# Kernel optimization log

Hardware: AMD Instinct MI355X
Metric: run time of the kernel (lower is better)

## Reference

```python
import jax, jax.numpy as jnp
import numpy as np

B, T, QL, KVL, D, H = 4, 512, 2, 1, 1024, 16
N = T * QL          # query tokens for self-attn
HD = D // H
MLP_H = 4 * D
EPS_ADA = 1e-6
EPS_LN = 1e-5
NEG = -10000.0


def _ln(x, eps):
    mu = jnp.mean(x, axis=-1, keepdims=True)
    xc = x - mu
    var = jnp.mean(xc * xc, axis=-1, keepdims=True)
    return xc * jax.lax.rsqrt(var + eps)


def _attention(xq, xk, xv, wq, wk, wv, wo, bo, mask, pad_add):
    # xq:[B,Nq,D] xk/xv:[B,Nk,D]; mask:[Nq,Nk] bool; pad_add:[B,1,1,Nk]
    qh = (xq @ wq).reshape(B, -1, H, HD).transpose(0, 2, 1, 3)
    kh = (xk @ wk).reshape(B, -1, H, HD).transpose(0, 2, 1, 3)
    vh = (xv @ wv).reshape(B, -1, H, HD).transpose(0, 2, 1, 3)
    dots = jnp.einsum('bhnd,bhmd->bhnm', qh, kh) * (HD ** -0.5)
    dots = jnp.where(mask[None, None], dots, jnp.asarray(NEG, dots.dtype))
    dots = dots + pad_add
    attn = jax.nn.softmax(dots, axis=-1)
    out = jnp.einsum('bhnm,bhmd->bhnd', attn, vh)
    out = out.transpose(0, 2, 1, 3).reshape(B, -1, D)
    return out @ wo + bo


def setup_inputs() -> dict:
    key = jax.random.key(0)
    ks = jax.random.split(key, 32)
    s = 0.02
    d = {
        'q': jax.random.normal(ks[0], (B, N, D), jnp.float32),
        'c': jax.random.normal(ks[1], (B, T, D), jnp.float32),
        'pe': jax.random.normal(ks[2], (B, T, D), jnp.float32),
        'padding_mask': jax.random.randint(ks[3], (B, T), 0, 2, jnp.int32),
        'w_mod': jax.random.normal(ks[4], (D, 6 * D), jnp.float32) * s,
        'b_mod': jnp.zeros((6 * D,), jnp.float32),
        'sa_wq': jax.random.normal(ks[5], (D, D), jnp.float32) * s,
        'sa_wk': jax.random.normal(ks[6], (D, D), jnp.float32) * s,
        'sa_wv': jax.random.normal(ks[7], (D, D), jnp.float32) * s,
        'sa_wo': jax.random.normal(ks[8], (D, D), jnp.float32) * s,
        'sa_bo': jnp.zeros((D,), jnp.float32),
        'ca_wq': jax.random.normal(ks[9], (D, D), jnp.float32) * s,
        'ca_wk': jax.random.normal(ks[10], (D, D), jnp.float32) * s,
        'ca_wv': jax.random.normal(ks[11], (D, D), jnp.float32) * s,
        'ca_wo': jax.random.normal(ks[12], (D, D), jnp.float32) * s,
        'ca_bo': jnp.zeros((D,), jnp.float32),
        'gk': jnp.ones((D,), jnp.float32), 'bk': jnp.zeros((D,), jnp.float32),
        'gv': jnp.ones((D,), jnp.float32), 'bv': jnp.zeros((D,), jnp.float32),
        'w_alpha': jax.random.normal(ks[13], (2 * D, D), jnp.float32) * s,
        'b_alpha': jnp.zeros((D,), jnp.float32),
        'w1': jax.random.normal(ks[14], (D, MLP_H), jnp.float32) * s,
        'b1': jnp.zeros((MLP_H,), jnp.float32),
        'w2': jax.random.normal(ks[15], (MLP_H, D), jnp.float32) * s,
        'b2': jnp.zeros((D,), jnp.float32),
    }
    return d


def reference(q, c, pe, padding_mask, w_mod, b_mod,
              sa_wq, sa_wk, sa_wv, sa_wo, sa_bo,
              ca_wq, ca_wk, ca_wv, ca_wo, ca_bo,
              gk, bk, gv, bv, w_alpha, b_alpha, w1, b1, w2, b2):
    # AdaLN modulation from condition c
    mod = jax.nn.silu(c) @ w_mod + b_mod                    # [B,T,6D]
    scale_sa, shift_sa, scale_ca, shift_ca, scale_mlp, shift_mlp = jnp.split(mod, 6, axis=2)
    rep = lambda t: jnp.repeat(t, QL, axis=1)               # [B,T,D]->[B,N,D]

    # masks
    causal = jnp.tril(jnp.ones((N, N), bool))
    tril_t = jnp.tril(jnp.ones((T, T), bool))
    cross_mask = jnp.repeat(jnp.repeat(tril_t, QL, axis=0), KVL, axis=1)  # [N, T*KVL]
    pad_f = padding_mask.astype(q.dtype)
    pad_sa = (jnp.repeat(pad_f, QL, axis=1) * NEG)[:, None, None, :]      # keys len N
    pad_ca = (jnp.repeat(pad_f, KVL, axis=1) * NEG)[:, None, None, :]     # keys len T

    # self-attention (pre-norm + modulation)
    q1 = _ln(q, EPS_ADA) * (1 + rep(scale_sa)) + rep(shift_sa)
    q1 = _attention(q1, q1, q1, sa_wq, sa_wk, sa_wv, sa_wo, sa_bo, causal, pad_sa)
    q = q1 + q

    # cross-attention with custom mask
    q2 = _ln(q, EPS_ADA) * (1 + rep(scale_ca)) + rep(shift_ca)
    kin = _ln(c + pe, EPS_LN) * gk + bk
    vin = _ln(c, EPS_LN) * gv + bv
    q2 = _attention(q2, kin, vin, ca_wq, ca_wk, ca_wv, ca_wo, ca_bo, cross_mask, pad_ca)
    alpha = jnp.concatenate([q2, q], axis=-1) @ w_alpha + b_alpha
    q = (1 + alpha) * q2 + q

    # MLP
    q3 = _ln(q, EPS_ADA) * (1 + rep(scale_mlp)) + rep(shift_mlp)
    h = jax.nn.gelu(q3 @ w1 + b1, approximate=False)
    q = q + (h @ w2 + b2)
    return q
```

## Files before the change

kernel.cpp:

```cpp
#include <hip/hip_runtime.h>
#include <cstdint>

typedef unsigned short u16;
typedef __attribute__((ext_vector_type(8))) short bf16x8;
typedef __attribute__((ext_vector_type(4))) float f32x4;

#define DEV static __device__ __forceinline__
#define AS1 __attribute__((address_space(1)))
#define AS3 __attribute__((address_space(3)))

static constexpr int Bb = 4, Tt = 512, Nn = 1024, Dd = 1024, Hh = 16;
static constexpr float NEGV = -10000.0f;

DEV u16 f2bf(float f) {
  unsigned int u = __builtin_bit_cast(unsigned int, f);
  u += 0x7fffu + ((u >> 16) & 1u);
  return (u16)(u >> 16);
}
DEV float bf2f(u16 s) {
  unsigned int u = ((unsigned int)s) << 16;
  return __builtin_bit_cast(float, u);
}
DEV f32x4 mfma16(bf16x8 a, bf16x8 b, f32x4 c) {
  return __builtin_amdgcn_mfma_f32_16x16x32_bf16(a, b, c, 0, 0, 0);
}
DEV void gload16(const u16* g, u16* lds) {
  __builtin_amdgcn_global_load_lds((AS1 const unsigned int*)g, (AS3 unsigned int*)lds, 16, 0, 0);
}
DEV int swz8(int wg, int nwg) { const int c = nwg >> 3; return (wg & 7) * c + (wg >> 3); }

__global__ __launch_bounds__(256) void transpose_cast(const float* __restrict__ src,
                                                      u16* __restrict__ dst, int R, int C) {
  __shared__ float tile[32][33];
  const int c0 = blockIdx.x * 32, r0 = blockIdx.y * 32;
  const int tx = threadIdx.x, ty = threadIdx.y;
#pragma unroll
  for (int j = 0; j < 4; ++j)
    tile[ty + 8 * j][tx] = src[(size_t)(r0 + ty + 8 * j) * C + c0 + tx];
  __syncthreads();
#pragma unroll
  for (int j = 0; j < 4; ++j)
    dst[(size_t)(c0 + ty + 8 * j) * R + r0 + tx] = f2bf(tile[tx][ty + 8 * j]);
}

__global__ __launch_bounds__(256) void silu_k(const float* __restrict__ c, u16* __restrict__ o, int n) {
  int i = blockIdx.x * 256 + threadIdx.x;
  if (i < n) { float x = c[i]; o[i] = f2bf(x / (1.0f + __expf(-x))); }
}

__global__ __launch_bounds__(256) void cat_k(const float* __restrict__ q2, const float* __restrict__ qr,
                                             u16* __restrict__ cat) {
  int i = blockIdx.x * 256 + threadIdx.x;
  int r = i >> 10, c = i & 1023;
  cat[(size_t)r * 2048 + c] = f2bf(q2[i]);
  cat[(size_t)r * 2048 + 1024 + c] = f2bf(qr[i]);
}

__global__ __launch_bounds__(256) void init_k(float* __restrict__ out, const float* __restrict__ bias,
                                              const float* __restrict__ res) {
  const int i = blockIdx.x * 256 + threadIdx.x;
  const float4 bv = ((const float4*)bias)[i & 255];
  float4 v = bv;
  if (res) {
    const float4 rv = ((const float4*)res)[i];
    v.x += rv.x; v.y += rv.y; v.z += rv.z; v.w += rv.w;
  }
  ((float4*)out)[i] = v;
}

__global__ __launch_bounds__(256) void comb_k(const float* __restrict__ alp, const float* __restrict__ q2,
                                              float* __restrict__ qres) {
  const int i = blockIdx.x * 256 + threadIdx.x;
  const float4 a = ((const float4*)alp)[i];
  const float4 b = ((const float4*)q2)[i];
  float4 r = ((float4*)qres)[i];
  r.x += (1.0f + a.x) * b.x; r.y += (1.0f + a.y) * b.y;
  r.z += (1.0f + a.z) * b.z; r.w += (1.0f + a.w) * b.w;
  ((float4*)qres)[i] = r;
}

__global__ __launch_bounds__(64) void mrow_k(const int* __restrict__ pm, float* __restrict__ M) {
  const int tid = threadIdx.x;
  const int b = tid >> 4, seg = tid & 15;
  int pre[32];
  int a = 1;
#pragma unroll
  for (int j = 0; j < 32; ++j) { a &= pm[b * 512 + seg * 32 + j]; pre[j] = a; }
  const int total = a;
  int excl = 1;
  for (int s = 0; s < 16; ++s) {
    int o = __shfl(total, (b << 4) + s, 64);
    if (s < seg) excl &= o;
  }
#pragma unroll
  for (int j = 0; j < 32; ++j)
    M[b * 512 + seg * 32 + j] = (excl & pre[j]) ? NEGV : 0.0f;
}

__global__ __launch_bounds__(256) void ln_mod_k(const float* __restrict__ X, const u16* __restrict__ MOD,
                                                u16* __restrict__ OUT, int chunk) {
  const int row = blockIdx.x;
  const int b = row >> 10, i = row & 1023, t = i >> 1;
  const int tid = threadIdx.x;
  const float4 xv = *(const float4*)&X[(size_t)row * 1024 + tid * 4];
  float s = xv.x + xv.y + xv.z + xv.w;
  float q = xv.x * xv.x + xv.y * xv.y + xv.z * xv.z + xv.w * xv.w;
#pragma unroll
  for (int off = 32; off > 0; off >>= 1) { s += __shfl_down(s, off); q += __shfl_down(q, off); }
  __shared__ float rs[4], rq[4];
  if ((tid & 63) == 0) { rs[tid >> 6] = s; rq[tid >> 6] = q; }
  __syncthreads();
  float S = rs[0] + rs[1] + rs[2] + rs[3];
  float Q = rq[0] + rq[1] + rq[2] + rq[3];
  const float mu = S * (1.0f / 1024.0f);
  const float var = Q * (1.0f / 1024.0f) - mu * mu;
  const float rstd = rsqrtf(var + 1e-6f);
  const u16* mrow = MOD + (size_t)(b * Tt + t) * 6144 + chunk * 1024 + tid * 4;
  u16* out = OUT + (size_t)row * 1024 + tid * 4;
  const float xx[4] = {xv.x, xv.y, xv.z, xv.w};
#pragma unroll
  for (int j = 0; j < 4; ++j) {
    float sc = bf2f(mrow[j]);
    float sh = bf2f(mrow[1024 + j]);
    out[j] = f2bf((xx[j] - mu) * rstd * (1.0f + sc) + sh);
  }
}

__global__ __launch_bounds__(256) void ln_kv_k(const float* __restrict__ C_, const float* __restrict__ PE,
                                               const float* __restrict__ gk, const float* __restrict__ bk,
                                               const float* __restrict__ gv, const float* __restrict__ bv,
                                               u16* __restrict__ KIN, u16* __restrict__ VIN) {
  const int row = blockIdx.x, tid = threadIdx.x;
  const size_t base = (size_t)row * 1024 + tid * 4;
  const float4 cv = *(const float4*)&C_[base];
  const float4 pv = *(const float4*)&PE[base];
  const float a[4] = {cv.x + pv.x, cv.y + pv.y, cv.z + pv.z, cv.w + pv.w};
  const float bb[4] = {cv.x, cv.y, cv.z, cv.w};
  float sa = a[0] + a[1] + a[2] + a[3];
  float qa = a[0] * a[0] + a[1] * a[1] + a[2] * a[2] + a[3] * a[3];
  float sb = bb[0] + bb[1] + bb[2] + bb[3];
  float qb = bb[0] * bb[0] + bb[1] * bb[1] + bb[2] * bb[2] + bb[3] * bb[3];
#pragma unroll
  for (int off = 32; off > 0; off >>= 1) {
    sa += __shfl_down(sa, off); qa += __shfl_down(qa, off);
    sb += __shfl_down(sb, off); qb += __shfl_down(qb, off);
  }
  __shared__ float r4[4][4];
  if ((tid & 63) == 0) {
    int w = tid >> 6;
    r4[0][w] = sa; r4[1][w] = qa; r4[2][w] = sb; r4[3][w] = qb;
  }
  __syncthreads();
  sa = r4[0][0] + r4[0][1] + r4[0][2] + r4[0][3];
  qa = r4[1][0] + r4[1][1] + r4[1][2] + r4[1][3];
  sb = r4[2][0] + r4[2][1] + r4[2][2] + r4[2][3];
  qb = r4[3][0] + r4[3][1] + r4[3][2] + r4[3][3];
  const float mua = sa * (1.0f / 1024.0f);
  const float ra = rsqrtf(qa * (1.0f / 1024.0f) - mua * mua + 1e-5f);
  const float mub = sb * (1.0f / 1024.0f);
  const float rb = rsqrtf(qb * (1.0f / 1024.0f) - mub * mub + 1e-5f);
#pragma unroll
  for (int j = 0; j < 4; ++j) {
    int d = tid * 4 + j;
    KIN[(size_t)row * 1024 + d] = f2bf((a[j] - mua) * ra * gk[d] + bk[d]);
    VIN[(size_t)row * 1024 + d] = f2bf((bb[j] - mub) * rb * gv[d] + bv[d]);
  }
}

DEV void stage32(const u16* __restrict__ A, const u16* __restrict__ Bt, int K,
                 int brow, int bcol, int kb, u16 (*As)[32], u16 (*Bs)[32]) {
  const int l = threadIdx.x & 63, wid = threadIdx.x >> 6;
#pragma unroll
  for (int p = 0; p < 2; ++p) {
    const int r0 = p * 64 + wid * 16;
    const int row = r0 + (l >> 2), kof = (l & 3) << 3;
    gload16(&A[(size_t)(brow + row) * K + kb + kof], &As[r0][0]);
    gload16(&Bt[(size_t)(bcol + row) * K + kb + kof], &Bs[r0][0]);
  }
}

DEV void gcore(const u16* __restrict__ A, const u16* __restrict__ Bt, int K,
               int brow, int bcol, int k0, int nk32,
               u16 (*As)[128][32], u16 (*Bs)[128][32], f32x4 (&acc)[4][4]) {
  const int l = threadIdx.x & 63, wid = threadIdx.x >> 6;
  const int wr = wid >> 1, wc = wid & 1;
  const int fr = l & 15, fg = l >> 4;
  stage32(A, Bt, K, brow, bcol, k0, As[0], Bs[0]);
  __syncthreads();
  int cur = 0;
  for (int kt = 0; kt < nk32; ++kt) {
    if (kt + 1 < nk32)
      stage32(A, Bt, K, brow, bcol, k0 + ((kt + 1) << 5), As[cur ^ 1], Bs[cur ^ 1]);
    bf16x8 af[4], bfr[4];
#pragma unroll
    for (int m = 0; m < 4; ++m) af[m] = *(const bf16x8*)&As[cur][wr * 64 + m * 16 + fr][fg * 8];
#pragma unroll
    for (int n = 0; n < 4; ++n) bfr[n] = *(const bf16x8*)&Bs[cur][wc * 64 + n * 16 + fr][fg * 8];
#pragma unroll
    for (int m = 0; m < 4; ++m)
#pragma unroll
      for (int n = 0; n < 4; ++n) acc[m][n] = mfma16(af[m], bfr[n], acc[m][n]);
    __syncthreads();
    cur ^= 1;
  }
}

template <int EPI>
__global__ __launch_bounds__(256) void gemm_k(const u16* __restrict__ A, const u16* __restrict__ Bt,
                                              int N, int K, const float* __restrict__ bias,
                                              u16* __restrict__ outb, int nbx) {
  __shared__ u16 As[2][128][32];
  __shared__ u16 Bs[2][128][32];
  const int wg = swz8(blockIdx.x, gridDim.x);
  const int brow = (wg / nbx) * 128, bcol = (wg % nbx) * 128;
  const int l = threadIdx.x & 63, wid = threadIdx.x >> 6;
  const int wr = wid >> 1, wc = wid & 1, fr = l & 15, fg = l >> 4;
  f32x4 acc[4][4];
#pragma unroll
  for (int m = 0; m < 4; ++m)
#pragma unroll
    for (int n = 0; n < 4; ++n) acc[m][n] = (f32x4){0.f, 0.f, 0.f, 0.f};
  gcore(A, Bt, K, brow, bcol, 0, K >> 5, As, Bs, acc);
#pragma unroll
  for (int m = 0; m < 4; ++m)
#pragma unroll
    for (int n = 0; n < 4; ++n)
#pragma unroll
      for (int r = 0; r < 4; ++r) {
        const int row = brow + wr * 64 + m * 16 + fg * 4 + r;
        const int col = bcol + wc * 64 + n * 16 + fr;
        float v = acc[m][n][r];
        if (EPI != 0) v += bias[col];
        if (EPI == 2) {
          const float u = v * (0.7978845608f + 0.0356774081f * v * v);
          v = v / (1.0f + __expf(-2.0f * u));
        }
        outb[(size_t)row * N + col] = f2bf(v);
      }
}

__global__ __launch_bounds__(256) void gemm_sk(const u16* __restrict__ A, const u16* __restrict__ Bt,
                                               int N, int K, float* __restrict__ outf, int nbx) {
  __shared__ u16 As[2][128][32];
  __shared__ u16 Bs[2][128][32];
  const int wg = swz8(blockIdx.x, gridDim.x);
  const int brow = (wg / nbx) * 128, bcol = (wg % nbx) * 128;
  const int half32 = K >> 6;
  const int k0 = blockIdx.y * (half32 << 5);
  const int l = threadIdx.x & 63, wid = threadIdx.x >> 6;
  const int wr = wid >> 1, wc = wid & 1, fr = l & 15, fg = l >> 4;
  f32x4 acc[4][4];
#pragma unroll
  for (int m = 0; m < 4; ++m)
#pragma unroll
    for (int n = 0; n < 4; ++n) acc[m][n] = (f32x4){0.f, 0.f, 0.f, 0.f};
  gcore(A, Bt, K, brow, bcol, k0, half32, As, Bs, acc);
#pragma unroll
  for (int m = 0; m < 4; ++m)
#pragma unroll
    for (int n = 0; n < 4; ++n)
#pragma unroll
      for (int r = 0; r < 4; ++r) {
        const int row = brow + wr * 64 + m * 16 + fg * 4 + r;
        const int col = bcol + wc * 64 + n * 16 + fr;
        atomicAdd(&outf[(size_t)row * N + col], acc[m][n][r]);
      }
}

__global__ __launch_bounds__(256) void gemm3_k(const u16* A0, const u16* A1, const u16* A2,
                                               const u16* B0, const u16* B1, const u16* B2,
                                               u16* O0, u16* O1, u16* O2) {
  const int z = blockIdx.y;
  const int wg = swz8(blockIdx.x, gridDim.x);
  const int bx = wg & 7, by = wg >> 3;
  if (z > 0 && by >= 16) return;
  const u16* A = z == 0 ? A0 : (z == 1 ? A1 : A2);
  const u16* Bt = z == 0 ? B0 : (z == 1 ? B1 : B2);
  u16* O = z == 0 ? O0 : (z == 1 ? O1 : O2);
  __shared__ u16 As[2][128][32];
  __shared__ u16 Bs[2][128][32];
  const int brow = by * 128, bcol = bx * 128;
  const int l = threadIdx.x & 63, wid = threadIdx.x >> 6;
  const int wr = wid >> 1, wc = wid & 1, fr = l & 15, fg = l >> 4;
  f32x4 acc[4][4];
#pragma unroll
  for (int m = 0; m < 4; ++m)
#pragma unroll
    for (int n = 0; n < 4; ++n) acc[m][n] = (f32x4){0.f, 0.f, 0.f, 0.f};
  gcore(A, Bt, 1024, brow, bcol, 0, 32, As, Bs, acc);
#pragma unroll
  for (int m = 0; m < 4; ++m)
#pragma unroll
    for (int n = 0; n < 4; ++n)
#pragma unroll
      for (int r = 0; r < 4; ++r) {
        const int row = brow + wr * 64 + m * 16 + fg * 4 + r;
        const int col = bcol + wc * 64 + n * 16 + fr;
        O[(size_t)row * 1024 + col] = f2bf(acc[m][n][r]);
      }
}

template <int QDIV, int PDIV>
__global__ __launch_bounds__(256) void attn_k(const u16* __restrict__ QH, const u16* __restrict__ KH,
                                              const u16* __restrict__ VH, u16* __restrict__ AO,
                                              const int* __restrict__ pmask, const float* __restrict__ Mrow,
                                              int Nq, int Nk, int qs, int ks) {
  __shared__ u16 Ks[32][72];
  __shared__ u16 Vt[64][40];
  __shared__ u16 Pl[4][16][40];
  const int tid = threadIdx.x;
  const int l = tid & 63, wid = tid >> 6;
  const int fr = l & 15, fg = l >> 4;
  const int nqb = Nq >> 6;
  const int wgid = swz8(blockIdx.x, gridDim.x);
  const int qb = wgid % nqb;
  const int bh = wgid / nqb;
  const int h = bh & 15, b = bh >> 4;
  const int q0 = qb * 64 + wid * 16;

  const size_t qrow = (size_t)(b * Nq + q0 + fr) * qs + h * 64;
  const bf16x8 aq0 = *(const bf16x8*)&QH[qrow + fg * 8];
  const bf16x8 aq1 = *(const bf16x8*)&QH[qrow + 32 + fg * 8];

  float Mr[4];
#pragma unroll
  for (int r = 0; r < 4; ++r) Mr[r] = Mrow[b * Tt + ((q0 + fg * 4 + r) >> 1)];

  f32x4 o[4];
#pragma unroll
  for (int c = 0; c < 4; ++c) o[c] = (f32x4){0.f, 0.f, 0.f, 0.f};
  float lsum[4] = {0.f, 0.f, 0.f, 0.f};

  int nkt = Nk >> 5;
  if (Mrow[b * Tt + ((qb * 64) >> 1)] == 0.0f) {
    const int kallow = (qb * 64 + 63) / QDIV + 1;
    const int t = (kallow + 31) >> 5;
    if (t < nkt) nkt = t;
  }

  const int srow = tid >> 3, skof = (tid & 7) << 3;
  for (int kt = 0; kt < nkt; ++kt) {
    const int kb = kt << 5;
    {
      const size_t g = (size_t)(b * Nk + kb + srow) * ks + h * 64 + skof;
      *(uint4*)&Ks[srow][skof] = *(const uint4*)&KH[g];
      union { uint4 u; u16 s[8]; } uv;
      uv.u = *(const uint4*)&VH[g];
#pragma unroll
      for (int j = 0; j < 8; ++j) Vt[skof + j][srow] = uv.s[j];
    }
    __syncthreads();

    f32x4 s0 = (f32x4){0.f, 0.f, 0.f, 0.f}, s1 = (f32x4){0.f, 0.f, 0.f, 0.f};
    {
      bf16x8 kf;
      kf = *(const bf16x8*)&Ks[fr][fg * 8];        s0 = mfma16(aq0, kf, s0);
      kf = *(const bf16x8*)&Ks[fr][32 + fg * 8];   s0 = mfma16(aq1, kf, s0);
      kf = *(const bf16x8*)&Ks[16 + fr][fg * 8];       s1 = mfma16(aq0, kf, s1);
      kf = *(const bf16x8*)&Ks[16 + fr][32 + fg * 8];  s1 = mfma16(aq1, kf, s1);
    }
    const int c0 = kb + fr, c1 = kb + 16 + fr;
    const float pad0 = pmask[b * Tt + (PDIV == 2 ? (c0 >> 1) : c0)] ? NEGV : 0.0f;
    const float pad1 = pmask[b * Tt + (PDIV == 2 ? (c1 >> 1) : c1)] ? NEGV : 0.0f;

#pragma unroll
    for (int r = 0; r < 4; ++r) {
      const int rq = (q0 + fg * 4 + r) >> (QDIV == 2 ? 1 : 0);
      float v0 = s0[r] * 0.125f; v0 = (c0 <= rq) ? v0 : NEGV; v0 += pad0;
      float v1 = s1[r] * 0.125f; v1 = (c1 <= rq) ? v1 : NEGV; v1 += pad1;
      const float p0 = __expf(v0 - Mr[r]);
      const float p1 = __expf(v1 - Mr[r]);
      lsum[r] += p0 + p1;
      Pl[wid][fg * 4 + r][fr] = f2bf(p0);
      Pl[wid][fg * 4 + r][16 + fr] = f2bf(p1);
    }

    const bf16x8 pa = *(const bf16x8*)&Pl[wid][fr][fg * 8];
#pragma unroll
    for (int c = 0; c < 4; ++c) {
      const bf16x8 vb = *(const bf16x8*)&Vt[c * 16 + fr][fg * 8];
      o[c] = mfma16(pa, vb, o[c]);
    }
    __syncthreads();
  }

#pragma unroll
  for (int r = 0; r < 4; ++r) {
    lsum[r] += __shfl_xor(lsum[r], 1);
    lsum[r] += __shfl_xor(lsum[r], 2);
    lsum[r] += __shfl_xor(lsum[r], 4);
    lsum[r] += __shfl_xor(lsum[r], 8);
  }

#pragma unroll
  for (int c = 0; c < 4; ++c)
#pragma unroll
    for (int r = 0; r < 4; ++r) {
      const int row = q0 + fg * 4 + r;
      AO[(size_t)(b * Nq + row) * Dd + h * 64 + c * 16 + fr] = f2bf(o[c][r] / lsum[r]);
    }
}

extern "C" void kernel_launch(void* const* d_in, const int* in_sizes, int n_in,
                              void* d_out, int out_size, void* d_ws, size_t ws_size,
                              hipStream_t stream) {
  (void)in_sizes; (void)n_in; (void)out_size; (void)ws_size;
  const float* q_in   = (const float*)d_in[0];
  const float* c_in   = (const float*)d_in[1];
  const float* pe     = (const float*)d_in[2];
  const int*   pmask  = (const int*)d_in[3];
  const float* w_mod  = (const float*)d_in[4];
  const float* b_mod  = (const float*)d_in[5];
  const float* sa_wq  = (const float*)d_in[6];
  const float* sa_wk  = (const float*)d_in[7];
  const float* sa_wv  = (const float*)d_in[8];
  const float* sa_wo  = (const float*)d_in[9];
  const float* sa_bo  = (const float*)d_in[10];
  const float* ca_wq  = (const float*)d_in[11];
  const float* ca_wk  = (const float*)d_in[12];
  const float* ca_wv  = (const float*)d_in[13];
  const float* ca_wo  = (const float*)d_in[14];
  const float* ca_bo  = (const float*)d_in[15];
  const float* gk     = (const float*)d_in[16];
  const float* bk     = (const float*)d_in[17];
  const float* gv     = (const float*)d_in[18];
  const float* bv     = (const float*)d_in[19];
  const float* w_alpha= (const float*)d_in[20];
  const float* b_alpha= (const float*)d_in[21];
  const float* w1     = (const float*)d_in[22];
  const float* b1     = (const float*)d_in[23];
  const float* w2     = (const float*)d_in[24];
  const float* b2     = (const float*)d_in[25];

  u16* ws = (u16*)d_ws;
  u16* WMODt  = ws + 0;
  float* Mp   = (float*)WMODt;
  u16* SAWQt  = ws + 6291456;
  u16* SAWKt  = ws + 7340032;
  u16* SAWVt  = ws + 8388608;
  u16* SAWOt  = ws + 9437184;
  u16* CAWQt  = ws + 10485760;
  u16* CAWKt  = ws + 11534336;
  u16* CAWVt  = ws + 12582912;
  u16* CAWOt  = ws + 13631488;
  u16* WALPHt = ws + 14680064;
  u16* W1t    = ws + 16777216;
  u16* W2t    = ws + 20971520;
  u16* Xs     = ws + 25165824;
  u16* KINp   = Xs;
  u16* VINp   = SAWQt;
  u16* MODbf  = ws + 27262976;
  u16* LNO    = ws + 39845888;
  u16* BIG    = ws + 44040192;
  u16* QKVp = BIG;
  u16* AOp  = BIG + 12582912;
  u16* CAQp = BIG;
  u16* CAKp = BIG + 4194304;
  u16* CAVp = BIG + 6291456;
  u16* AO2p = BIG + 8388608;
  u16* CATp = BIG;
  float* ALPf = (float*)(BIG + 8388608);
  u16* HBp  = BIG;
  float* Qres = (float*)(ws + 60817408);
  float* Q2f  = Qres + 4194304;
  float* outp = (float*)d_out;

  const dim3 blk(256);
  auto TR = [&](const float* s, u16* d, int R, int C) {
    transpose_cast<<<dim3(C / 32, R / 32), dim3(32, 8), 0, stream>>>(s, d, R, C);
  };

  TR(w_mod, WMODt, 1024, 6144);
  TR(sa_wq, SAWQt, 1024, 1024); TR(sa_wk, SAWKt, 1024, 1024);
  TR(sa_wv, SAWVt, 1024, 1024); TR(sa_wo, SAWOt, 1024, 1024);
  TR(ca_wq, CAWQt, 1024, 1024); TR(ca_wk, CAWKt, 1024, 1024);
  TR(ca_wv, CAWVt, 1024, 1024); TR(ca_wo, CAWOt, 1024, 1024);
  TR(w_alpha, WALPHt, 2048, 1024);
  TR(w1, W1t, 1024, 4096);
  TR(w2, W2t, 4096, 1024);

  silu_k<<<8192, blk, 0, stream>>>(c_in, Xs, 2048 * 1024);
  gemm_k<1><<<768, blk, 0, stream>>>(Xs, WMODt, 6144, 1024, b_mod, MODbf, 48);
  mrow_k<<<1, 64, 0, stream>>>(pmask, Mp);

  ln_mod_k<<<4096, blk, 0, stream>>>(q_in, MODbf, LNO, 0);
  gemm_k<0><<<768, blk, 0, stream>>>(LNO, SAWQt, 3072, 1024, nullptr, QKVp, 24);
  ln_kv_k<<<2048, blk, 0, stream>>>(c_in, pe, gk, bk, gv, bv, KINp, VINp);
  attn_k<1, 2><<<1024, blk, 0, stream>>>(QKVp, QKVp + 1024, QKVp + 2048, AOp, pmask, Mp,
                                         1024, 1024, 3072, 3072);
  init_k<<<4096, blk, 0, stream>>>(Qres, sa_bo, q_in);
  gemm_sk<<<dim3(256, 2), blk, 0, stream>>>(AOp, SAWOt, 1024, 1024, Qres, 8);

  ln_mod_k<<<4096, blk, 0, stream>>>(Qres, MODbf, LNO, 2);
  gemm3_k<<<dim3(256, 3), blk, 0, stream>>>(LNO, KINp, VINp, CAWQt, CAWKt, CAWVt, CAQp, CAKp, CAVp);
  attn_k<2, 1><<<1024, blk, 0, stream>>>(CAQp, CAKp, CAVp, AO2p, pmask, Mp,
                                         1024, 512, 1024, 1024);
  init_k<<<4096, blk, 0, stream>>>(Q2f, ca_bo, nullptr);
  gemm_sk<<<dim3(256, 2), blk, 0, stream>>>(AO2p, CAWOt, 1024, 1024, Q2f, 8);
  cat_k<<<16384, blk, 0, stream>>>(Q2f, Qres, CATp);
  init_k<<<4096, blk, 0, stream>>>(ALPf, b_alpha, nullptr);
  gemm_sk<<<dim3(256, 2), blk, 0, stream>>>(CATp, WALPHt, 1024, 2048, ALPf, 8);
  comb_k<<<4096, blk, 0, stream>>>(ALPf, Q2f, Qres);

  ln_mod_k<<<4096, blk, 0, stream>>>(Qres, MODbf, LNO, 4);
  gemm_k<2><<<1024, blk, 0, stream>>>(LNO, W1t, 4096, 1024, b1, HBp, 32);
  init_k<<<4096, blk, 0, stream>>>(outp, b2, Qres);
  gemm_sk<<<dim3(256, 2), blk, 0, stream>>>(HBp, W2t, 1024, 4096, outp, 8);
}
```

Measured before the change: 576.4 us.

## Write V transposed from projection GEMMs and use per-wave swizzled LDS in attention

The QKV and cross-attention projection GEMMs now write V directly in a transposed [B, D, Nk] layout. The attention kernel can then load V tiles with direct global-to-LDS loads instead of doing a scalar transpose through shared memory. Each wave gets its own XOR-swizzled K and V LDS buffers filled with gload16, so the block-wide __syncthreads is replaced by a per-wave vmcnt wait. The cost is scattered, uncoalesced stores in the GEMM epilogue for V and more LDS per block. Each wave also loads its own redundant copy of the K/V tiles, which raises global traffic.

```diff
diff --git a/kernel.cpp b/kernel.cpp
--- a/kernel.cpp
+++ b/kernel.cpp
@@ -239,6 +239,34 @@
       }
 }
 
+__global__ __launch_bounds__(256) void gemm_qkv(const u16* __restrict__ A, const u16* __restrict__ Bt,
+                                                u16* __restrict__ qk, u16* __restrict__ vt) {
+  __shared__ u16 As[2][128][32];
+  __shared__ u16 Bs[2][128][32];
+  const int wg = swz8(blockIdx.x, gridDim.x);
+  const int brow = (wg / 24) * 128, bcol = (wg % 24) * 128;
+  const int l = threadIdx.x & 63, wid = threadIdx.x >> 6;
+  const int wr = wid >> 1, wc = wid & 1, fr = l & 15, fg = l >> 4;
+  f32x4 acc[4][4];
+#pragma unroll
+  for (int m = 0; m < 4; ++m)
+#pragma unroll
+    for (int n = 0; n < 4; ++n) acc[m][n] = (f32x4){0.f, 0.f, 0.f, 0.f};
+  gcore(A, Bt, 1024, brow, bcol, 0, 32, As, Bs, acc);
+#pragma unroll
+  for (int m = 0; m < 4; ++m)
+#pragma unroll
+    for (int n = 0; n < 4; ++n)
+#pragma unroll
+      for (int r = 0; r < 4; ++r) {
+        const int row = brow + wr * 64 + m * 16 + fg * 4 + r;
+        const int col = bcol + wc * 64 + n * 16 + fr;
+        const u16 v = f2bf(acc[m][n][r]);
+        if (col < 2048) qk[(size_t)row * 2048 + col] = v;
+        else vt[(size_t)(row >> 10) * 1048576 + (size_t)(col - 2048) * 1024 + (row & 1023)] = v;
+      }
+}
+
 __global__ __launch_bounds__(256) void gemm_sk(const u16* __restrict__ A, const u16* __restrict__ Bt,
                                                int N, int K, float* __restrict__ outf, int nbx) {
   __shared__ u16 As[2][128][32];
@@ -269,14 +297,13 @@
 
 __global__ __launch_bounds__(256) void gemm3_k(const u16* A0, const u16* A1, const u16* A2,
                                                const u16* B0, const u16* B1, const u16* B2,
-                                               u16* O0, u16* O1, u16* O2) {
+                                               u16* O0, u16* O1, u16* VT2) {
   const int z = blockIdx.y;
   const int wg = swz8(blockIdx.x, gridDim.x);
   const int bx = wg & 7, by = wg >> 3;
   if (z > 0 && by >= 16) return;
   const u16* A = z == 0 ? A0 : (z == 1 ? A1 : A2);
   const u16* Bt = z == 0 ? B0 : (z == 1 ? B1 : B2);
-  u16* O = z == 0 ? O0 : (z == 1 ? O1 : O2);
   __shared__ u16 As[2][128][32];
   __shared__ u16 Bs[2][128][32];
   const int brow = by * 128, bcol = bx * 128;
@@ -296,18 +323,20 @@
       for (int r = 0; r < 4; ++r) {
         const int row = brow + wr * 64 + m * 16 + fg * 4 + r;
         const int col = bcol + wc * 64 + n * 16 + fr;
-        O[(size_t)row * 1024 + col] = f2bf(acc[m][n][r]);
+        const u16 v = f2bf(acc[m][n][r]);
+        if (z == 2) VT2[(size_t)(row >> 9) * 524288 + (size_t)col * 512 + (row & 511)] = v;
+        else (z == 0 ? O0 : O1)[(size_t)row * 1024 + col] = v;
       }
 }
 
 template <int QDIV, int PDIV>
 __global__ __launch_bounds__(256) void attn_k(const u16* __restrict__ QH, const u16* __restrict__ KH,
-                                              const u16* __restrict__ VH, u16* __restrict__ AO,
+                                              const u16* __restrict__ VT, u16* __restrict__ AO,
                                               const int* __restrict__ pmask, const float* __restrict__ Mrow,
                                               int Nq, int Nk, int qs, int ks) {
-  __shared__ u16 Ks[32][72];
-  __shared__ u16 Vt[64][40];
-  __shared__ u16 Pl[4][16][40];
+  __shared__ u16 KS[4][2048];
+  __shared__ u16 VS[4][2048];
+  __shared__ u16 PL[4][16][40];
   const int tid = threadIdx.x;
   const int l = tid & 63, wid = tid >> 6;
   const int fr = l & 15, fg = l >> 4;
@@ -318,6 +347,15 @@
   const int h = bh & 15, b = bh >> 4;
   const int q0 = qb * 64 + wid * 16;
 
+  u16* Ksl = KS[wid];
+  u16* Vsl = VS[wid];
+  u16 (*Pl)[40] = PL[wid];
+
+  const int krow = l >> 3;
+  const int kslot = (l & 7) ^ krow;
+  const int vrow = l >> 2;
+  const int vslot = (l & 3) ^ (vrow & 3);
+
   const size_t qrow = (size_t)(b * Nq + q0 + fr) * qs + h * 64;
   const bf16x8 aq0 = *(const bf16x8*)&QH[qrow + fg * 8];
   const bf16x8 aq1 = *(const bf16x8*)&QH[qrow + 32 + fg * 8];
@@ -338,26 +376,27 @@
     if (t < nkt) nkt = t;
   }
 
-  const int srow = tid >> 3, skof = (tid & 7) << 3;
+  const int sw0 = (fg ^ (fr & 7)) * 8;
+  const int sw1 = ((4 + fg) ^ (fr & 7)) * 8;
+  const size_t vtb = (size_t)b * 1024 * Nk + (size_t)(h * 64) * Nk;
+
   for (int kt = 0; kt < nkt; ++kt) {
     const int kb = kt << 5;
-    {
-      const size_t g = (size_t)(b * Nk + kb + srow) * ks + h * 64 + skof;
-      *(uint4*)&Ks[srow][skof] = *(const uint4*)&KH[g];
-      union { uint4 u; u16 s[8]; } uv;
-      uv.u = *(const uint4*)&VH[g];
-#pragma unroll
-      for (int j = 0; j < 8; ++j) Vt[skof + j][srow] = uv.s[j];
+#pragma unroll
+    for (int p = 0; p < 4; ++p) {
+      gload16(&KH[(size_t)(b * Nk + kb + p * 8 + krow) * ks + h * 64 + kslot * 8], &Ksl[p * 512]);
+      gload16(&VT[vtb + (size_t)(p * 16 + vrow) * Nk + kb + vslot * 8], &Vsl[p * 512]);
     }
-    __syncthreads();
+    asm volatile("s_waitcnt vmcnt(0)" ::: "memory");
+    __builtin_amdgcn_sched_barrier(0);
 
     f32x4 s0 = (f32x4){0.f, 0.f, 0.f, 0.f}, s1 = (f32x4){0.f, 0.f, 0.f, 0.f};
     {
       bf16x8 kf;
-      kf = *(const bf16x8*)&Ks[fr][fg * 8];        s0 = mfma16(aq0, kf, s0);
-      kf = *(const bf16x8*)&Ks[fr][32 + fg * 8];   s0 = mfma16(aq1, kf, s0);
-      kf = *(const bf16x8*)&Ks[16 + fr][fg * 8];       s1 = mfma16(aq0, kf, s1);
-      kf = *(const bf16x8*)&Ks[16 + fr][32 + fg * 8];  s1 = mfma16(aq1, kf, s1);
+      kf = *(const bf16x8*)&Ksl[fr * 64 + sw0];        s0 = mfma16(aq0, kf, s0);
+      kf = *(const bf16x8*)&Ksl[fr * 64 + sw1];        s0 = mfma16(aq1, kf, s0);
+      kf = *(const bf16x8*)&Ksl[(16 + fr) * 64 + sw0]; s1 = mfma16(aq0, kf, s1);
+      kf = *(const bf16x8*)&Ksl[(16 + fr) * 64 + sw1]; s1 = mfma16(aq1, kf, s1);
     }
     const int c0 = kb + fr, c1 = kb + 16 + fr;
     const float pad0 = pmask[b * Tt + (PDIV == 2 ? (c0 >> 1) : c0)] ? NEGV : 0.0f;
@@ -371,17 +410,16 @@
       const float p0 = __expf(v0 - Mr[r]);
       const float p1 = __expf(v1 - Mr[r]);
       lsum[r] += p0 + p1;
-      Pl[wid][fg * 4 + r][fr] = f2bf(p0);
-      Pl[wid][fg * 4 + r][16 + fr] = f2bf(p1);
+      Pl[fg * 4 + r][fr] = f2bf(p0);
+      Pl[fg * 4 + r][16 + fr] = f2bf(p1);
     }
 
-    const bf16x8 pa = *(const bf16x8*)&Pl[wid][fr][fg * 8];
+    const bf16x8 pa = *(const bf16x8*)&Pl[fr][fg * 8];
 #pragma unroll
     for (int c = 0; c < 4; ++c) {
-      const bf16x8 vb = *(const bf16x8*)&Vt[c * 16 + fr][fg * 8];
+      const bf16x8 vb = *(const bf16x8*)&Vsl[(c * 16 + fr) * 32 + ((fg ^ (fr & 3)) << 3)];
       o[c] = mfma16(pa, vb, o[c]);
     }
-    __syncthreads();
   }
 
 #pragma unroll
@@ -452,13 +490,14 @@
   u16* MODbf  = ws + 27262976;
   u16* LNO    = ws + 39845888;
   u16* BIG    = ws + 44040192;
-  u16* QKVp = BIG;
-  u16* AOp  = BIG + 12582912;
-  u16* CAQp = BIG;
-  u16* CAKp = BIG + 4194304;
-  u16* CAVp = BIG + 6291456;
-  u16* AO2p = BIG + 8388608;
-  u16* CATp = BIG;
+  u16* QKp   = BIG;
+  u16* VTsa  = BIG + 8388608;
+  u16* AOp   = BIG + 12582912;
+  u16* CAQp  = BIG;
+  u16* CAKp  = BIG + 4194304;
+  u16* VT2   = BIG + 6291456;
+  u16* AO2p  = BIG + 8388608;
+  u16* CATp  = BIG;
   float* ALPf = (float*)(BIG + 8388608);
   u16* HBp  = BIG;
   float* Qres = (float*)(ws + 60817408);
@@ -484,16 +523,16 @@
   mrow_k<<<1, 64, 0, stream>>>(pmask, Mp);
 
   ln_mod_k<<<4096, blk, 0, stream>>>(q_in, MODbf, LNO, 0);
-  gemm_k<0><<<768, blk, 0, stream>>>(LNO, SAWQt, 3072, 1024, nullptr, QKVp, 24);
+  gemm_qkv<<<768, blk, 0, stream>>>(LNO, SAWQt, QKp, VTsa);
   ln_kv_k<<<2048, blk, 0, stream>>>(c_in, pe, gk, bk, gv, bv, KINp, VINp);
-  attn_k<1, 2><<<1024, blk, 0, stream>>>(QKVp, QKVp + 1024, QKVp + 2048, AOp, pmask, Mp,
-                                         1024, 1024, 3072, 3072);
+  attn_k<1, 2><<<1024, blk, 0, stream>>>(QKp, QKp + 1024, VTsa, AOp, pmask, Mp,
+                                         1024, 1024, 2048, 2048);
   init_k<<<4096, blk, 0, stream>>>(Qres, sa_bo, q_in);
   gemm_sk<<<dim3(256, 2), blk, 0, stream>>>(AOp, SAWOt, 1024, 1024, Qres, 8);
 
   ln_mod_k<<<4096, blk, 0, stream>>>(Qres, MODbf, LNO, 2);
-  gemm3_k<<<dim3(256, 3), blk, 0, stream>>>(LNO, KINp, VINp, CAWQt, CAWKt, CAWVt, CAQp, CAKp, CAVp);
-  attn_k<2, 1><<<1024, blk, 0, stream>>>(CAQp, CAKp, CAVp, AO2p, pmask, Mp,
+  gemm3_k<<<dim3(256, 3), blk, 0, stream>>>(LNO, KINp, VINp, CAWQt, CAWKt, CAWVt, CAQp, CAKp, VT2);
+  attn_k<2, 1><<<1024, blk, 0, stream>>>(CAQp, CAKp, VT2, AO2p, pmask, Mp,
                                          1024, 512, 1024, 1024);
   init_k<<<4096, blk, 0, stream>>>(Q2f, ca_bo, nullptr);
   gemm_sk<<<dim3(256, 2), blk, 0, stream>>>(AO2p, CAWOt, 1024, 1024, Q2f, 8);
```

Result: no change. 580.3 us (+0.7%).
